# Performance work log

Measured on AMD Instinct MI355X. Metric: run time of the kernel, lower is better.

Reference implementation:

```python
import jax, jax.numpy as jnp
import numpy as np

B, L, D, H, E = 64, 128, 768, 2, 131072  # graphs, nodes/graph, hidden, heads, edges
N = B * L
C = D // H  # per-head channels


def _transformer_conv(x, src, dst, wq, bq, wk, bk, wv, bv, ws, bs):
    # PyG TransformerConv (concat=True, root_weight=True, beta=False)
    n = x.shape[0]
    q = (x @ wq + bq).reshape(n, H, C)
    k = (x @ wk + bk).reshape(n, H, C)
    v = (x @ wv + bv).reshape(n, H, C)
    # per-edge attention logits [E, H]
    logits = jnp.sum(q[dst] * k[src], axis=-1) * (1.0 / np.sqrt(C))
    # scatter softmax over incoming edges of each dst node
    m = jax.ops.segment_max(logits, dst, num_segments=n)
    e = jnp.exp(logits - m[dst])
    s = jax.ops.segment_sum(e, dst, num_segments=n)
    alpha = e / s[dst]  # [E, H]
    msg = alpha[..., None] * v[src]  # [E, H, C]
    agg = jax.ops.segment_sum(msg, dst, num_segments=n).reshape(n, D)
    return agg + x @ ws + bs


def setup_inputs() -> dict:
    key = jax.random.key(0)
    ks = jax.random.split(key, 24)
    x = jax.random.normal(ks[0], (N, D), jnp.float32)
    # within-graph random edges
    dst = jax.random.randint(ks[1], (E,), 0, N)
    off = jax.random.randint(ks[2], (E,), 0, L)
    src = (dst // L) * L + off
    edge_index = jnp.stack([src, dst]).astype(jnp.int32)

    def lin(k, i, o):
        return jax.random.normal(k, (i, o), jnp.float32) * 0.02

    inp = {"x": x, "edge_index": edge_index}
    i = 3
    for layer in ("1", "2"):
        for nm in ("wq", "wk", "wv", "ws"):
            inp[nm + layer] = lin(ks[i], D, D); i += 1
            inp["b" + nm[1] + layer] = jnp.zeros((D,), jnp.float32)
    inp["atti_w"] = lin(ks[i], 2 * D, D); i += 1
    inp["atti_b"] = jnp.zeros((D,), jnp.float32)
    inp["atts_w"] = lin(ks[i], D, 1); i += 1
    inp["atts_b"] = jnp.zeros((1,), jnp.float32)
    inp["fc1_w"] = lin(ks[i], D, D); i += 1
    inp["fc1_b"] = jnp.zeros((D,), jnp.float32)
    inp["fc2_w"] = lin(ks[i], D, 3); i += 1
    inp["fc2_b"] = jnp.zeros((3,), jnp.float32)
    return inp


def reference(x, edge_index, wq1, bq1, wk1, bk1, wv1, bv1, ws1, bs1,
              wq2, bq2, wk2, bk2, wv2, bv2, ws2, bs2,
              atti_w, atti_b, atts_w, atts_b, fc1_w, fc1_b, fc2_w, fc2_b):
    src, dst = edge_index[0], edge_index[1]
    h = jax.nn.relu(_transformer_conv(x, src, dst, wq1, bq1, wk1, bk1, wv1, bv1, ws1, bs1))
    h = jax.nn.relu(_transformer_conv(h, src, dst, wq2, bq2, wk2, bk2, wv2, bv2, ws2, bs2))
    # pad(): equal-size graphs -> reshape, mask all-valid (x_mask all False)
    hp = h.reshape(B, L, D)
    # attention pooling (eval path): query = first node of each graph
    x_q = jnp.broadcast_to(hp[:, :1], hp.shape)  # [B, L, D]
    x_c = jax.nn.relu(jnp.concatenate([x_q, hp], axis=-1) @ atti_w + atti_b)
    score = x_c @ atts_w + atts_b  # [B, L, 1]
    score = jax.nn.softmax(score, axis=1)
    pooled = jnp.sum(hp * score, axis=1)  # [B, D]
    out = jnp.tanh(pooled @ fc1_w + fc1_b) @ fc2_w + fc2_b
    return jax.nn.log_softmax(out, axis=-1)
```

## Files before the change

kernel.cpp:

```cpp
#include <hip/hip_runtime.h>

#define NN 8192
#define DD 768
#define EE 131072
#define BBg 64
#define LLn 128
#define CCh 384

typedef unsigned short u16;
typedef unsigned char u8;
typedef __attribute__((ext_vector_type(8))) short short8;
typedef __attribute__((ext_vector_type(4))) float f32x4;

__device__ __forceinline__ float b2f(u16 u) {
    union { unsigned int i; float f; } x; x.i = ((unsigned int)u) << 16; return x.f;
}
__device__ __forceinline__ u16 f2b(float f) {
    union { float f; unsigned int i; } x; x.f = f;
    unsigned int r = x.i + 0x7fffu + ((x.i >> 16) & 1u);
    return (u16)(r >> 16);
}
__device__ __forceinline__ void gload16(const void* g, void* l) {
    __builtin_amdgcn_global_load_lds((const __attribute__((address_space(1))) void*)g,
                                     (__attribute__((address_space(3))) void*)l, 16, 0, 0);
}

__global__ void cnt_build(const int* __restrict__ srcp, const int* __restrict__ dstp,
                          unsigned int* __restrict__ cnt32) {
    int e = blockIdx.x * 256 + threadIdx.x;
    int d = dstp[e], s = srcp[e];
    int g = d >> 7;
    int idx = (g << 14) + ((d & 127) << 7) + (s & 127);
    atomicAdd(&cnt32[idx >> 2], 1u << ((idx & 3) * 8));
}

__global__ void f32_to_bf16_vec(const float* __restrict__ in, u16* __restrict__ out, int n4) {
    int i = blockIdx.x * 256 + threadIdx.x;
    if (i >= n4) return;
    float4 v = ((const float4*)in)[i];
    ushort4 o; o.x = f2b(v.x); o.y = f2b(v.y); o.z = f2b(v.z); o.w = f2b(v.w);
    ((ushort4*)out)[i] = o;
}

struct TP { const float* src; u16* dst; int rowOff; };
struct TP11 { TP a[11]; };

__global__ __launch_bounds__(256) void transpose_batched(TP11 args) {
    __shared__ float tile[64][65];
    TP tp = args.a[blockIdx.z];
    int n0 = blockIdx.x * 64, k0 = blockIdx.y * 64;
    int t = threadIdx.x;
    int tc = t & 63, tr = t >> 6;
#pragma unroll
    for (int i = 0; i < 16; i++)
        tile[tr + i * 4][tc] = tp.src[(size_t)(tp.rowOff + k0 + tr + i * 4) * DD + n0 + tc];
    __syncthreads();
#pragma unroll
    for (int i = 0; i < 16; i++) {
        int row = tr + i * 4;
        tp.dst[(size_t)(n0 + row) * DD + k0 + tc] = f2b(tile[tc][row]);
    }
}

__global__ void gather_first(const u16* __restrict__ hb2, u16* __restrict__ hq) {
    int idx = blockIdx.x * 256 + threadIdx.x;
    int b = idx / DD;
    int c = idx - b * DD;
    hq[idx] = hb2[(size_t)(b * LLn) * DD + c];
}

enum { EPI_F32 = 1, EPI_TANH = 3 };

__global__ __launch_bounds__(256) void gemm_bf16(const u16* __restrict__ A,
                                                 const u16* __restrict__ Wt,
                                                 const float* __restrict__ bias,
                                                 void* __restrict__ outp, int K, int mode) {
    __shared__ u16 As[64][72];
    __shared__ u16 Bs[64][72];
    const int m0 = blockIdx.y * 64, n0 = blockIdx.x * 64;
    const int t = threadIdx.x;
    const int lane = t & 63, w = t >> 6;
    const int tr = t >> 2, tc = (t & 3) * 16;
    f32x4 acc[4] = {{0,0,0,0},{0,0,0,0},{0,0,0,0},{0,0,0,0}};
    const int fRow = lane & 15;
    const int fK = (lane >> 4) * 8;

    for (int k0 = 0; k0 < K; k0 += 64) {
        int4 a0 = *(const int4*)(A + (size_t)(m0 + tr) * K + k0 + tc);
        int4 a1 = *(const int4*)(A + (size_t)(m0 + tr) * K + k0 + tc + 8);
        int4 b0 = *(const int4*)(Wt + (size_t)(n0 + tr) * K + k0 + tc);
        int4 b1 = *(const int4*)(Wt + (size_t)(n0 + tr) * K + k0 + tc + 8);
        __syncthreads();
        *(int4*)&As[tr][tc] = a0; *(int4*)&As[tr][tc + 8] = a1;
        *(int4*)&Bs[tr][tc] = b0; *(int4*)&Bs[tr][tc + 8] = b1;
        __syncthreads();
#pragma unroll
        for (int s = 0; s < 2; s++) {
            short8 af = *(const short8*)&As[w * 16 + fRow][s * 32 + fK];
#pragma unroll
            for (int g = 0; g < 4; g++) {
                short8 bf = *(const short8*)&Bs[g * 16 + fRow][s * 32 + fK];
                acc[g] = __builtin_amdgcn_mfma_f32_16x16x32_bf16(af, bf, acc[g], 0, 0, 0);
            }
        }
    }
    const int colLocal = lane & 15;
    const int rowLocal = (lane >> 4) * 4;
#pragma unroll
    for (int g = 0; g < 4; g++) {
        int col = n0 + g * 16 + colLocal;
        float bv = bias ? bias[col] : 0.f;
#pragma unroll
        for (int i = 0; i < 4; i++) {
            int row = m0 + w * 16 + rowLocal + i;
            float v = acc[g][i] + bv;
            if (mode == EPI_TANH) v = tanhf(v);
            ((float*)outp)[(size_t)row * DD + col] = v;
        }
    }
}

enum { MODE_QKVS = 0, MODE_XC = 1 };

__global__ __launch_bounds__(256) void gemm128(const u16* __restrict__ A,
                                               const u16* __restrict__ Wt, int K,
                                               const float* __restrict__ b0,
                                               const float* __restrict__ b1,
                                               const float* __restrict__ b2,
                                               const float* __restrict__ b3,
                                               void* __restrict__ o0, void* __restrict__ o1,
                                               void* __restrict__ o2, void* __restrict__ o3,
                                               const float* __restrict__ aq, int mode) {
    __shared__ u16 As[128 * 64];
    __shared__ u16 Bs[128 * 64];
    const int t = threadIdx.x;
    const int lane = t & 63, w = t >> 6;
    const int wr = w >> 1, wc = w & 1;
    const int m0 = blockIdx.y * 128, n0 = blockIdx.x * 128;
    const int fRow = lane & 15, fThr = lane >> 4;
    f32x4 acc[4][4] = {};
    const u16* Abase = A + (size_t)m0 * K;
    const u16* Bbase = Wt + (size_t)n0 * K;

    for (int k0 = 0; k0 < K; k0 += 64) {
        __syncthreads();
#pragma unroll
        for (int i = 0; i < 4; i++) {
            int c = t + 256 * i;
            int row = c >> 3;
            int col = (((c & 7) ^ (row & 7))) * 8;
            gload16(Abase + (size_t)row * K + k0 + col, (char*)As + (size_t)c * 16);
            gload16(Bbase + (size_t)row * K + k0 + col, (char*)Bs + (size_t)c * 16);
        }
        __syncthreads();
#pragma unroll
        for (int kk = 0; kk < 64; kk += 32) {
            const int cjW = (kk >> 3) + fThr;
            short8 af[4], bf[4];
#pragma unroll
            for (int i = 0; i < 4; i++) {
                int R = wr * 64 + i * 16 + fRow;
                af[i] = *(const short8*)&As[(R * 8 + (cjW ^ (R & 7))) * 8];
            }
#pragma unroll
            for (int g = 0; g < 4; g++) {
                int R = wc * 64 + g * 16 + fRow;
                bf[g] = *(const short8*)&Bs[(R * 8 + (cjW ^ (R & 7))) * 8];
            }
#pragma unroll
            for (int i = 0; i < 4; i++)
#pragma unroll
                for (int g = 0; g < 4; g++)
                    acc[i][g] = __builtin_amdgcn_mfma_f32_16x16x32_bf16(af[i], bf[g], acc[i][g], 0, 0, 0);
        }
    }
    if (mode == MODE_XC) {
        float* scoreOut = (float*)o0;
        const float* aw = b1;
        const int cb2 = n0 + wc * 64;
        float rsum[4][4] = {};
#pragma unroll
        for (int g = 0; g < 4; g++) {
            int col = cb2 + g * 16 + fRow;
            float bv = b0[col], av = aw[col];
#pragma unroll
            for (int i = 0; i < 4; i++) {
                int rowb = m0 + wr * 64 + i * 16 + fThr * 4;
#pragma unroll
                for (int rr = 0; rr < 4; rr++) {
                    int row = rowb + rr;
                    float v = fmaxf(acc[i][g][rr] + bv + aq[(size_t)(row >> 7) * DD + col], 0.f);
                    rsum[i][rr] += v * av;
                }
            }
        }
#pragma unroll
        for (int i = 0; i < 4; i++)
#pragma unroll
            for (int rr = 0; rr < 4; rr++) {
                float s = rsum[i][rr];
                s += __shfl_xor(s, 1, 16); s += __shfl_xor(s, 2, 16);
                s += __shfl_xor(s, 4, 16); s += __shfl_xor(s, 8, 16);
                if (fRow == 0)
                    atomicAdd(&scoreOut[m0 + wr * 64 + i * 16 + fThr * 4 + rr], s);
            }
        return;
    }
    int chunk = (n0 + wc * 64) / DD;
    const float* bp = (chunk == 0) ? b0 : (chunk == 1) ? b1 : (chunk == 2) ? b2 : b3;
    void* op = (chunk == 0) ? o0 : (chunk == 1) ? o1 : (chunk == 2) ? o2 : o3;
    const int cb = n0 + wc * 64 - chunk * DD;
    if (chunk == 2) {
        u16* vt = (u16*)op;
#pragma unroll
        for (int g = 0; g < 4; g++) {
            int col = cb + g * 16 + fRow;
            float bv = bp[col];
#pragma unroll
            for (int i = 0; i < 4; i++) {
                int rowb = m0 + wr * 64 + i * 16 + fThr * 4;
                ushort4 st;
                st.x = f2b(acc[i][g][0] + bv);
                st.y = f2b(acc[i][g][1] + bv);
                st.z = f2b(acc[i][g][2] + bv);
                st.w = f2b(acc[i][g][3] + bv);
                *(ushort4*)(vt + (size_t)col * NN + rowb) = st;
            }
        }
    } else {
#pragma unroll
        for (int g = 0; g < 4; g++) {
            int col = cb + g * 16 + fRow;
            float bv = bp[col];
#pragma unroll
            for (int i = 0; i < 4; i++) {
                int rowb = m0 + wr * 64 + i * 16 + fThr * 4;
#pragma unroll
                for (int rr = 0; rr < 4; rr++) {
                    int row = rowb + rr;
                    ((u16*)op)[(size_t)row * DD + col] = f2b(acc[i][g][rr] + bv);
                }
            }
        }
    }
}

__global__ __launch_bounds__(256) void attn_fused(const u16* __restrict__ qb,
                                                  const u16* __restrict__ kb,
                                                  const u16* __restrict__ vT,
                                                  const u8* __restrict__ cnt,
                                                  const u16* __restrict__ hs,
                                                  u16* __restrict__ out) {
    __shared__ u16 As[64][72];
    __shared__ u16 Bs[128][72];
    __shared__ u16 Pl[64][136];
    __shared__ u16 Vt[64][136];
    const int half = blockIdx.x, hd = blockIdx.y, g = blockIdx.z;
    const int t = threadIdx.x;
    const int lane = t & 63, w = t >> 6;
    const int fRow = lane & 15, fThr = lane >> 4;
    const int dstBase = g * 128 + half * 64;
    const u16* Qb = qb + (size_t)dstBase * DD + hd * CCh;
    const u16* Kb = kb + (size_t)(g * 128) * DD + hd * CCh;

    f32x4 acc[8] = {};
    const int trA = t >> 2, tcA = (t & 3) * 16;
    const int trB = t >> 1, tcB = (t & 1) * 32;
    for (int k0 = 0; k0 < CCh; k0 += 64) {
        int4 a0 = *(const int4*)(Qb + (size_t)trA * DD + k0 + tcA);
        int4 a1 = *(const int4*)(Qb + (size_t)trA * DD + k0 + tcA + 8);
        int4 b0 = *(const int4*)(Kb + (size_t)trB * DD + k0 + tcB);
        int4 b1 = *(const int4*)(Kb + (size_t)trB * DD + k0 + tcB + 8);
        int4 b2 = *(const int4*)(Kb + (size_t)trB * DD + k0 + tcB + 16);
        int4 b3 = *(const int4*)(Kb + (size_t)trB * DD + k0 + tcB + 24);
        __syncthreads();
        *(int4*)&As[trA][tcA] = a0; *(int4*)&As[trA][tcA + 8] = a1;
        *(int4*)&Bs[trB][tcB] = b0; *(int4*)&Bs[trB][tcB + 8] = b1;
        *(int4*)&Bs[trB][tcB + 16] = b2; *(int4*)&Bs[trB][tcB + 24] = b3;
        __syncthreads();
#pragma unroll
        for (int kk = 0; kk < 64; kk += 32) {
            short8 af = *(const short8*)&As[w * 16 + fRow][kk + fThr * 8];
#pragma unroll
            for (int j = 0; j < 8; j++) {
                short8 bf = *(const short8*)&Bs[j * 16 + fRow][kk + fThr * 8];
                acc[j] = __builtin_amdgcn_mfma_f32_16x16x32_bf16(af, bf, acc[j], 0, 0, 0);
            }
        }
    }

    const float scale = 0.05103103630798288f;
    const u8* cg = cnt + ((size_t)g << 14);
    const int rbase = half * 64 + w * 16 + fThr * 4;
    float pv[8][4];
#pragma unroll
    for (int i = 0; i < 4; i++) {
        float m = -3.4e38f;
#pragma unroll
        for (int j = 0; j < 8; j++) {
            float c = (float)cg[(rbase + i) * 128 + j * 16 + fRow];
            float s = acc[j][i] * scale;
            pv[j][i] = c;
            if (c > 0.f) m = fmaxf(m, s);
        }
#pragma unroll
        for (int msk = 1; msk <= 8; msk <<= 1) m = fmaxf(m, __shfl_xor(m, msk, 16));
        float sum = 0.f;
#pragma unroll
        for (int j = 0; j < 8; j++) {
            float p = (pv[j][i] > 0.f) ? pv[j][i] * __expf(acc[j][i] * scale - m) : 0.f;
            pv[j][i] = p; sum += p;
        }
#pragma unroll
        for (int msk = 1; msk <= 8; msk <<= 1) sum += __shfl_xor(sum, msk, 16);
        float inv = (sum > 0.f) ? 1.f / sum : 0.f;
#pragma unroll
        for (int j = 0; j < 8; j++)
            Pl[w * 16 + fThr * 4 + i][j * 16 + fRow] = f2b(pv[j][i] * inv);
    }

    for (int cc = 0; cc < 6; cc++) {
        __syncthreads();
#pragma unroll
        for (int ii = 0; ii < 4; ii++) {
            int q = t + 256 * ii;
            int row = q >> 4, col = (q & 15) * 8;
            *(int4*)&Vt[row][col] =
                *(const int4*)(vT + (size_t)(hd * CCh + cc * 64 + row) * NN + g * 128 + col);
        }
        __syncthreads();
        f32x4 acc2[4] = {};
#pragma unroll
        for (int kk = 0; kk < 128; kk += 32) {
            short8 af = *(const short8*)&Pl[w * 16 + fRow][kk + fThr * 8];
#pragma unroll
            for (int j = 0; j < 4; j++) {
                short8 bf = *(const short8*)&Vt[j * 16 + fRow][kk + fThr * 8];
                acc2[j] = __builtin_amdgcn_mfma_f32_16x16x32_bf16(af, bf, acc2[j], 0, 0, 0);
            }
        }
#pragma unroll
        for (int j = 0; j < 4; j++) {
            int c = hd * CCh + cc * 64 + j * 16 + fRow;
#pragma unroll
            for (int i = 0; i < 4; i++) {
                int row = dstBase + w * 16 + fThr * 4 + i;
                size_t idx = (size_t)row * DD + c;
                float r = fmaxf(acc2[j][i] + b2f(hs[idx]), 0.f);
                out[idx] = f2b(r);
            }
        }
    }
}

__global__ __launch_bounds__(192) void pool_kernel(const float* __restrict__ score,
                                                   const u16* __restrict__ hx,
                                                   float* __restrict__ pooled) {
    int b = blockIdx.x, t = threadIdx.x;
    __shared__ float sprob[LLn];
    if (t < 64) {
        float s0 = score[b * LLn + t];
        float s1 = score[b * LLn + 64 + t];
        float mx = fmaxf(s0, s1);
#pragma unroll
        for (int m = 1; m <= 32; m <<= 1) mx = fmaxf(mx, __shfl_xor(mx, m, 64));
        float e0 = __expf(s0 - mx), e1 = __expf(s1 - mx);
        float sum = e0 + e1;
#pragma unroll
        for (int m = 1; m <= 32; m <<= 1) sum += __shfl_xor(sum, m, 64);
        float inv = 1.f / sum;
        sprob[t] = e0 * inv; sprob[t + 64] = e1 * inv;
    }
    __syncthreads();
    int c = t * 4;
    float a0 = 0, a1 = 0, a2 = 0, a3 = 0;
    for (int l = 0; l < LLn; l++) {
        float wl = sprob[l];
        ushort4 hv = *(const ushort4*)(hx + (size_t)(b * LLn + l) * DD + c);
        a0 += wl * b2f(hv.x); a1 += wl * b2f(hv.y); a2 += wl * b2f(hv.z); a3 += wl * b2f(hv.w);
    }
    float4 o; o.x = a0; o.y = a1; o.z = a2; o.w = a3;
    *(float4*)(pooled + (size_t)b * DD + c) = o;
}

__global__ __launch_bounds__(256) void head2_kernel(const float* __restrict__ u,
                                                    const float* __restrict__ fc2w,
                                                    const float* __restrict__ fc2b,
                                                    float* __restrict__ outp) {
    int b = blockIdx.x, t = threadIdx.x;
    __shared__ float sred[4][3];
    float p0 = 0, p1 = 0, p2 = 0;
    for (int k = t; k < DD; k += 256) {
        float uv = u[(size_t)b * DD + k];
        p0 += uv * fc2w[k * 3 + 0]; p1 += uv * fc2w[k * 3 + 1]; p2 += uv * fc2w[k * 3 + 2];
    }
#pragma unroll
    for (int m = 1; m <= 32; m <<= 1) {
        p0 += __shfl_xor(p0, m, 64); p1 += __shfl_xor(p1, m, 64); p2 += __shfl_xor(p2, m, 64);
    }
    int w = t >> 6, lane = t & 63;
    if (lane == 0) { sred[w][0] = p0; sred[w][1] = p1; sred[w][2] = p2; }
    __syncthreads();
    if (t == 0) {
        float z0 = fc2b[0], z1 = fc2b[1], z2 = fc2b[2];
        for (int i = 0; i < 4; i++) { z0 += sred[i][0]; z1 += sred[i][1]; z2 += sred[i][2]; }
        float mx = fmaxf(z0, fmaxf(z1, z2));
        float lse = mx + logf(__expf(z0 - mx) + __expf(z1 - mx) + __expf(z2 - mx));
        outp[b * 3 + 0] = z0 - lse; outp[b * 3 + 1] = z1 - lse; outp[b * 3 + 2] = z2 - lse;
    }
}

static inline char* carve(char*& p, size_t bytes) {
    char* r = p;
    p += (bytes + 255) & ~(size_t)255;
    return r;
}

extern "C" void kernel_launch(void* const* d_in, const int* in_sizes, int n_in,
                              void* d_out, int out_size, void* d_ws, size_t ws_size,
                              hipStream_t stream) {
    const float* x = (const float*)d_in[0];
    const int* ei = (const int*)d_in[1];
    const int* srcp = ei;
    const int* dstp = ei + EE;
    const float* wL[8] = {(const float*)d_in[2], (const float*)d_in[4], (const float*)d_in[6],
                          (const float*)d_in[8], (const float*)d_in[10], (const float*)d_in[12],
                          (const float*)d_in[14], (const float*)d_in[16]};
    const float* bL[8] = {(const float*)d_in[3], (const float*)d_in[5], (const float*)d_in[7],
                          (const float*)d_in[9], (const float*)d_in[11], (const float*)d_in[13],
                          (const float*)d_in[15], (const float*)d_in[17]};
    const float* atti_w = (const float*)d_in[18];
    const float* atti_b = (const float*)d_in[19];
    const float* atts_w = (const float*)d_in[20];
    const float* fc1_w = (const float*)d_in[22];
    const float* fc1_b = (const float*)d_in[23];
    const float* fc2_w = (const float*)d_in[24];
    const float* fc2_b = (const float*)d_in[25];
    float* outp = (float*)d_out;

    char* p = (char*)d_ws;
    const size_t ndb = (size_t)NN * DD * 2;
    const size_t wsz = (size_t)DD * DD * 2;
    u16* qb = (u16*)carve(p, ndb);
    u16* kb = (u16*)carve(p, ndb);
    u16* vt = (u16*)carve(p, ndb);
    u16* xb = (u16*)carve(p, ndb);
    u16* hb = (u16*)carve(p, ndb);
    u16* hs = (u16*)carve(p, ndb);
    u16* wtcat1 = (u16*)carve(p, wsz * 4);
    u16* wtcat2 = (u16*)carve(p, wsz * 4);
    u16* wt8 = (u16*)carve(p, wsz);
    u16* wt9 = (u16*)carve(p, wsz);
    u16* wtfc1 = (u16*)carve(p, wsz);
    u16* hq = (u16*)carve(p, (size_t)BBg * DD * 2);
    u16* pb = (u16*)carve(p, (size_t)BBg * DD * 2);
    float* Aq = (float*)carve(p, (size_t)BBg * DD * 4);
    float* pooled = (float*)carve(p, (size_t)BBg * DD * 4);
    float* uu = (float*)carve(p, (size_t)BBg * DD * 4);
    u8* cnt = (u8*)carve(p, (size_t)BBg * 128 * 128);
    float* score = (float*)carve(p, NN * 4);

    hipMemsetAsync(cnt, 0, (size_t)BBg * 128 * 128, stream);
    hipMemsetAsync(score, 0, NN * 4, stream);
    cnt_build<<<EE / 256, 256, 0, stream>>>(srcp, dstp, (unsigned int*)cnt);

    f32_to_bf16_vec<<<(NN * DD / 4) / 256, 256, 0, stream>>>(x, xb, NN * DD / 4);
    TP11 tps;
    for (int i = 0; i < 4; i++) tps.a[i] = {wL[i], wtcat1 + (size_t)i * DD * DD, 0};
    for (int i = 0; i < 4; i++) tps.a[4 + i] = {wL[4 + i], wtcat2 + (size_t)i * DD * DD, 0};
    tps.a[8] = {atti_w, wt8, 0};
    tps.a[9] = {atti_w, wt9, DD};
    tps.a[10] = {fc1_w, wtfc1, 0};
    transpose_batched<<<dim3(12, 12, 11), 256, 0, stream>>>(tps);

    dim3 gf(24, 64);
    dim3 ga(2, 2, BBg);
    gemm128<<<gf, 256, 0, stream>>>(xb, wtcat1, DD, bL[0], bL[1], bL[2], bL[3],
                                    qb, kb, vt, hs, nullptr, MODE_QKVS);
    attn_fused<<<ga, 256, 0, stream>>>(qb, kb, vt, cnt, hs, hb);
    gemm128<<<gf, 256, 0, stream>>>(hb, wtcat2, DD, bL[4], bL[5], bL[6], bL[7],
                                    qb, kb, vt, hs, nullptr, MODE_QKVS);
    attn_fused<<<ga, 256, 0, stream>>>(qb, kb, vt, cnt, hs, xb);

    gather_first<<<(BBg * DD) / 256, 256, 0, stream>>>(xb, hq);
    gemm_bf16<<<dim3(12, 1), 256, 0, stream>>>(hq, wt8, nullptr, Aq, DD, EPI_F32);
    gemm128<<<dim3(6, 64), 256, 0, stream>>>(xb, wt9, DD, atti_b, atts_w, nullptr, nullptr,
                                             score, nullptr, nullptr, nullptr, Aq, MODE_XC);
    pool_kernel<<<BBg, 192, 0, stream>>>(score, xb, pooled);

    f32_to_bf16_vec<<<(BBg * DD / 4 + 255) / 256, 256, 0, stream>>>(pooled, pb, BBg * DD / 4);
    gemm_bf16<<<dim3(12, 1), 256, 0, stream>>>(pb, wtfc1, fc1_b, uu, DD, EPI_TANH);
    head2_kernel<<<BBg, 256, 0, stream>>>(uu, fc2_w, fc2_b, outp);
}
```

Baseline: 359.7 us.

## Enlarge QKVS GEMM tile to 256 rows and fuse pooling-query projection into xc GEMM

```diff
diff --git a/kernel.cpp b/kernel.cpp
--- a/kernel.cpp
+++ b/kernel.cpp
@@ -60,13 +60,6 @@
         int row = tr + i * 4;
         tp.dst[(size_t)(n0 + row) * DD + k0 + tc] = f2b(tile[tc][row]);
     }
-}
-
-__global__ void gather_first(const u16* __restrict__ hb2, u16* __restrict__ hq) {
-    int idx = blockIdx.x * 256 + threadIdx.x;
-    int b = idx / DD;
-    int c = idx - b * DD;
-    hq[idx] = hb2[(size_t)(b * LLn) * DD + c];
 }
 
 enum { EPI_F32 = 1, EPI_TANH = 3 };
@@ -120,46 +113,50 @@
     }
 }
 
-enum { MODE_QKVS = 0, MODE_XC = 1 };
-
-__global__ __launch_bounds__(256) void gemm128(const u16* __restrict__ A,
-                                               const u16* __restrict__ Wt, int K,
-                                               const float* __restrict__ b0,
-                                               const float* __restrict__ b1,
-                                               const float* __restrict__ b2,
-                                               const float* __restrict__ b3,
-                                               void* __restrict__ o0, void* __restrict__ o1,
-                                               void* __restrict__ o2, void* __restrict__ o3,
-                                               const float* __restrict__ aq, int mode) {
-    __shared__ u16 As[128 * 64];
+__global__ __launch_bounds__(256, 2) void gemm256(const u16* __restrict__ A,
+                                                  const u16* __restrict__ Wt,
+                                                  const float* __restrict__ b0,
+                                                  const float* __restrict__ b1,
+                                                  const float* __restrict__ b2,
+                                                  const float* __restrict__ b3,
+                                                  u16* __restrict__ o0, u16* __restrict__ o1,
+                                                  u16* __restrict__ o2, u16* __restrict__ o3) {
+    __shared__ u16 As[256 * 64];
     __shared__ u16 Bs[128 * 64];
+    const int K = DD;
     const int t = threadIdx.x;
     const int lane = t & 63, w = t >> 6;
     const int wr = w >> 1, wc = w & 1;
-    const int m0 = blockIdx.y * 128, n0 = blockIdx.x * 128;
+    const int m0 = blockIdx.y * 256, n0 = blockIdx.x * 128;
     const int fRow = lane & 15, fThr = lane >> 4;
-    f32x4 acc[4][4] = {};
+    f32x4 acc[8][4] = {};
     const u16* Abase = A + (size_t)m0 * K;
     const u16* Bbase = Wt + (size_t)n0 * K;
 
     for (int k0 = 0; k0 < K; k0 += 64) {
         __syncthreads();
+#pragma unroll
+        for (int i = 0; i < 8; i++) {
+            int c = t + 256 * i;
+            int row = c >> 3;
+            int col = ((c & 7) ^ (row & 7)) * 8;
+            gload16(Abase + (size_t)row * K + k0 + col, (char*)As + (size_t)c * 16);
+        }
 #pragma unroll
         for (int i = 0; i < 4; i++) {
             int c = t + 256 * i;
             int row = c >> 3;
-            int col = (((c & 7) ^ (row & 7))) * 8;
-            gload16(Abase + (size_t)row * K + k0 + col, (char*)As + (size_t)c * 16);
+            int col = ((c & 7) ^ (row & 7)) * 8;
             gload16(Bbase + (size_t)row * K + k0 + col, (char*)Bs + (size_t)c * 16);
         }
         __syncthreads();
 #pragma unroll
         for (int kk = 0; kk < 64; kk += 32) {
             const int cjW = (kk >> 3) + fThr;
-            short8 af[4], bf[4];
-#pragma unroll
-            for (int i = 0; i < 4; i++) {
-                int R = wr * 64 + i * 16 + fRow;
+            short8 af[8], bf[4];
+#pragma unroll
+            for (int i = 0; i < 8; i++) {
+                int R = wr * 128 + i * 16 + fRow;
                 af[i] = *(const short8*)&As[(R * 8 + (cjW ^ (R & 7))) * 8];
             }
 #pragma unroll
@@ -168,63 +165,30 @@
                 bf[g] = *(const short8*)&Bs[(R * 8 + (cjW ^ (R & 7))) * 8];
             }
 #pragma unroll
-            for (int i = 0; i < 4; i++)
+            for (int i = 0; i < 8; i++)
 #pragma unroll
                 for (int g = 0; g < 4; g++)
                     acc[i][g] = __builtin_amdgcn_mfma_f32_16x16x32_bf16(af[i], bf[g], acc[i][g], 0, 0, 0);
         }
     }
-    if (mode == MODE_XC) {
-        float* scoreOut = (float*)o0;
-        const float* aw = b1;
-        const int cb2 = n0 + wc * 64;
-        float rsum[4][4] = {};
-#pragma unroll
-        for (int g = 0; g < 4; g++) {
-            int col = cb2 + g * 16 + fRow;
-            float bv = b0[col], av = aw[col];
-#pragma unroll
-            for (int i = 0; i < 4; i++) {
-                int rowb = m0 + wr * 64 + i * 16 + fThr * 4;
-#pragma unroll
-                for (int rr = 0; rr < 4; rr++) {
-                    int row = rowb + rr;
-                    float v = fmaxf(acc[i][g][rr] + bv + aq[(size_t)(row >> 7) * DD + col], 0.f);
-                    rsum[i][rr] += v * av;
-                }
-            }
-        }
-#pragma unroll
-        for (int i = 0; i < 4; i++)
-#pragma unroll
-            for (int rr = 0; rr < 4; rr++) {
-                float s = rsum[i][rr];
-                s += __shfl_xor(s, 1, 16); s += __shfl_xor(s, 2, 16);
-                s += __shfl_xor(s, 4, 16); s += __shfl_xor(s, 8, 16);
-                if (fRow == 0)
-                    atomicAdd(&scoreOut[m0 + wr * 64 + i * 16 + fThr * 4 + rr], s);
-            }
-        return;
-    }
-    int chunk = (n0 + wc * 64) / DD;
+    const int chunk = (n0 + wc * 64) / DD;
     const float* bp = (chunk == 0) ? b0 : (chunk == 1) ? b1 : (chunk == 2) ? b2 : b3;
-    void* op = (chunk == 0) ? o0 : (chunk == 1) ? o1 : (chunk == 2) ? o2 : o3;
+    u16* op = (chunk == 0) ? o0 : (chunk == 1) ? o1 : (chunk == 2) ? o2 : o3;
     const int cb = n0 + wc * 64 - chunk * DD;
     if (chunk == 2) {
-        u16* vt = (u16*)op;
 #pragma unroll
         for (int g = 0; g < 4; g++) {
             int col = cb + g * 16 + fRow;
             float bv = bp[col];
 #pragma unroll
-            for (int i = 0; i < 4; i++) {
-                int rowb = m0 + wr * 64 + i * 16 + fThr * 4;
+            for (int i = 0; i < 8; i++) {
+                int rowb = m0 + wr * 128 + i * 16 + fThr * 4;
                 ushort4 st;
                 st.x = f2b(acc[i][g][0] + bv);
                 st.y = f2b(acc[i][g][1] + bv);
                 st.z = f2b(acc[i][g][2] + bv);
                 st.w = f2b(acc[i][g][3] + bv);
-                *(ushort4*)(vt + (size_t)col * NN + rowb) = st;
+                *(ushort4*)(op + (size_t)col * NN + rowb) = st;
             }
         }
     } else {
@@ -233,16 +197,107 @@
             int col = cb + g * 16 + fRow;
             float bv = bp[col];
 #pragma unroll
+            for (int i = 0; i < 8; i++) {
+                int rowb = m0 + wr * 128 + i * 16 + fThr * 4;
+#pragma unroll
+                for (int rr = 0; rr < 4; rr++)
+                    op[(size_t)(rowb + rr) * DD + col] = f2b(acc[i][g][rr] + bv);
+            }
+        }
+    }
+}
+
+__global__ __launch_bounds__(256) void gemm_xc(const u16* __restrict__ A,
+                                               const u16* __restrict__ Wt,
+                                               const u16* __restrict__ wt8,
+                                               const float* __restrict__ atti_b,
+                                               const float* __restrict__ atts_w,
+                                               float* __restrict__ score) {
+    __shared__ u16 As[128 * 64];
+    __shared__ u16 Bs[128 * 64];
+    __shared__ float aq_p[2][128];
+    const int K = DD;
+    const int t = threadIdx.x;
+    const int lane = t & 63, w = t >> 6;
+    const int wr = w >> 1, wc = w & 1;
+    const int n0 = blockIdx.x * 128, m0 = blockIdx.y * 128;
+    const int fRow = lane & 15, fThr = lane >> 4;
+
+    {
+        int col = t & 127, kh = t >> 7;
+        const u16* xr = A + (size_t)m0 * DD + kh * 384;
+        const u16* wr8 = wt8 + (size_t)(n0 + col) * DD + kh * 384;
+        float s = 0.f;
+#pragma unroll 8
+        for (int j = 0; j < 96; j++) {
+            ushort4 a4 = *(const ushort4*)(xr + j * 4);
+            ushort4 b4 = *(const ushort4*)(wr8 + j * 4);
+            s += b2f(a4.x) * b2f(b4.x) + b2f(a4.y) * b2f(b4.y)
+               + b2f(a4.z) * b2f(b4.z) + b2f(a4.w) * b2f(b4.w);
+        }
+        aq_p[kh][col] = s;
+    }
+
+    f32x4 acc[4][4] = {};
+    const u16* Abase = A + (size_t)m0 * K;
+    const u16* Bbase = Wt + (size_t)n0 * K;
+    for (int k0 = 0; k0 < K; k0 += 64) {
+        __syncthreads();
+#pragma unroll
+        for (int i = 0; i < 4; i++) {
+            int c = t + 256 * i;
+            int row = c >> 3;
+            int col = ((c & 7) ^ (row & 7)) * 8;
+            gload16(Abase + (size_t)row * K + k0 + col, (char*)As + (size_t)c * 16);
+            gload16(Bbase + (size_t)row * K + k0 + col, (char*)Bs + (size_t)c * 16);
+        }
+        __syncthreads();
+#pragma unroll
+        for (int kk = 0; kk < 64; kk += 32) {
+            const int cjW = (kk >> 3) + fThr;
+            short8 af[4], bf[4];
+#pragma unroll
             for (int i = 0; i < 4; i++) {
-                int rowb = m0 + wr * 64 + i * 16 + fThr * 4;
-#pragma unroll
-                for (int rr = 0; rr < 4; rr++) {
-                    int row = rowb + rr;
-                    ((u16*)op)[(size_t)row * DD + col] = f2b(acc[i][g][rr] + bv);
-                }
-            }
-        }
-    }
+                int R = wr * 64 + i * 16 + fRow;
+                af[i] = *(const short8*)&As[(R * 8 + (cjW ^ (R & 7))) * 8];
+            }
+#pragma unroll
+            for (int g = 0; g < 4; g++) {
+                int R = wc * 64 + g * 16 + fRow;
+                bf[g] = *(const short8*)&Bs[(R * 8 + (cjW ^ (R & 7))) * 8];
+            }
+#pragma unroll
+            for (int i = 0; i < 4; i++)
+#pragma unroll
+                for (int g = 0; g < 4; g++)
+                    acc[i][g] = __builtin_amdgcn_mfma_f32_16x16x32_bf16(af[i], bf[g], acc[i][g], 0, 0, 0);
+        }
+    }
+    float rsum[4][4] = {};
+#pragma unroll
+    for (int g = 0; g < 4; g++) {
+        int cl = wc * 64 + g * 16 + fRow;
+        int col = n0 + cl;
+        float bv = atti_b[col] + aq_p[0][cl] + aq_p[1][cl];
+        float av = atts_w[col];
+#pragma unroll
+        for (int i = 0; i < 4; i++)
+#pragma unroll
+            for (int rr = 0; rr < 4; rr++) {
+                float v = fmaxf(acc[i][g][rr] + bv, 0.f);
+                rsum[i][rr] += v * av;
+            }
+    }
+#pragma unroll
+    for (int i = 0; i < 4; i++)
+#pragma unroll
+        for (int rr = 0; rr < 4; rr++) {
+            float s = rsum[i][rr];
+            s += __shfl_xor(s, 1, 16); s += __shfl_xor(s, 2, 16);
+            s += __shfl_xor(s, 4, 16); s += __shfl_xor(s, 8, 16);
+            if (fRow == 0)
+                atomicAdd(&score[m0 + wr * 64 + i * 16 + fThr * 4 + rr], s);
+        }
 }
 
 __global__ __launch_bounds__(256) void attn_fused(const u16* __restrict__ qb,
@@ -355,7 +410,7 @@
 
 __global__ __launch_bounds__(192) void pool_kernel(const float* __restrict__ score,
                                                    const u16* __restrict__ hx,
-                                                   float* __restrict__ pooled) {
+                                                   u16* __restrict__ pb) {
     int b = blockIdx.x, t = threadIdx.x;
     __shared__ float sprob[LLn];
     if (t < 64) {
@@ -379,8 +434,8 @@
         ushort4 hv = *(const ushort4*)(hx + (size_t)(b * LLn + l) * DD + c);
         a0 += wl * b2f(hv.x); a1 += wl * b2f(hv.y); a2 += wl * b2f(hv.z); a3 += wl * b2f(hv.w);
     }
-    float4 o; o.x = a0; o.y = a1; o.z = a2; o.w = a3;
-    *(float4*)(pooled + (size_t)b * DD + c) = o;
+    ushort4 o; o.x = f2b(a0); o.y = f2b(a1); o.z = f2b(a2); o.w = f2b(a3);
+    *(ushort4*)(pb + (size_t)b * DD + c) = o;
 }
 
 __global__ __launch_bounds__(256) void head2_kernel(const float* __restrict__ u,
@@ -452,10 +507,7 @@
     u16* wt8 = (u16*)carve(p, wsz);
     u16* wt9 = (u16*)carve(p, wsz);
     u16* wtfc1 = (u16*)carve(p, wsz);
-    u16* hq = (u16*)carve(p, (size_t)BBg * DD * 2);
     u16* pb = (u16*)carve(p, (size_t)BBg * DD * 2);
-    float* Aq = (float*)carve(p, (size_t)BBg * DD * 4);
-    float* pooled = (float*)carve(p, (size_t)BBg * DD * 4);
     float* uu = (float*)carve(p, (size_t)BBg * DD * 4);
     u8* cnt = (u8*)carve(p, (size_t)BBg * 128 * 128);
     float* score = (float*)carve(p, NN * 4);
@@ -473,22 +525,16 @@
     tps.a[10] = {fc1_w, wtfc1, 0};
     transpose_batched<<<dim3(12, 12, 11), 256, 0, stream>>>(tps);
 
-    dim3 gf(24, 64);
+    dim3 gf(24, 32);
     dim3 ga(2, 2, BBg);
-    gemm128<<<gf, 256, 0, stream>>>(xb, wtcat1, DD, bL[0], bL[1], bL[2], bL[3],
-                                    qb, kb, vt, hs, nullptr, MODE_QKVS);
+    gemm256<<<gf, 256, 0, stream>>>(xb, wtcat1, bL[0], bL[1], bL[2], bL[3], qb, kb, vt, hs);
     attn_fused<<<ga, 256, 0, stream>>>(qb, kb, vt, cnt, hs, hb);
-    gemm128<<<gf, 256, 0, stream>>>(hb, wtcat2, DD, bL[4], bL[5], bL[6], bL[7],
-                                    qb, kb, vt, hs, nullptr, MODE_QKVS);
+    gemm256<<<gf, 256, 0, stream>>>(hb, wtcat2, bL[4], bL[5], bL[6], bL[7], qb, kb, vt, hs);
     attn_fused<<<ga, 256, 0, stream>>>(qb, kb, vt, cnt, hs, xb);
 
-    gather_first<<<(BBg * DD) / 256, 256, 0, stream>>>(xb, hq);
-    gemm_bf16<<<dim3(12, 1), 256, 0, stream>>>(hq, wt8, nullptr, Aq, DD, EPI_F32);
-    gemm128<<<dim3(6, 64), 256, 0, stream>>>(xb, wt9, DD, atti_b, atts_w, nullptr, nullptr,
-                                             score, nullptr, nullptr, nullptr, Aq, MODE_XC);
-    pool_kernel<<<BBg, 192, 0, stream>>>(score, xb, pooled);
-
-    f32_to_bf16_vec<<<(BBg * DD / 4 + 255) / 256, 256, 0, stream>>>(pooled, pb, BBg * DD / 4);
+    gemm_xc<<<dim3(6, 64), 256, 0, stream>>>(xb, wt9, wt8, atti_b, atts_w, score);
+    pool_kernel<<<BBg, 192, 0, stream>>>(score, xb, pb);
+
     gemm_bf16<<<dim3(12, 1), 256, 0, stream>>>(pb, wtfc1, fc1_b, uu, DD, EPI_TANH);
     head2_kernel<<<BBg, 256, 0, stream>>>(uu, fc2_w, fc2_b, outp);
 }
```

Result: faster. 352.3 us (-2.1%).
